# Kernel optimization log

Hardware: AMD Instinct MI355X
Metric: run time of the kernel (lower is better)

The kernel has to match this reference:

```python
import jax, jax.numpy as jnp
import numpy as np

C = 512
B, W, H = 16, 64, 64
K = 128


def setup_inputs() -> dict:
    key = jax.random.key(0)
    ks = jax.random.split(key, 17)
    s = 0.02
    inp = {
        "x1": jax.random.normal(ks[0], (B, C, W, H), jnp.float32),
        "y1": jax.random.normal(ks[1], (B, K, C), jnp.float32),
        "x2": jax.random.normal(ks[2], (B, C, W, H), jnp.float32),
        "y2": jax.random.normal(ks[3], (B, K, C), jnp.float32),
        # 1x1 conv weights stored as [out, in]
        "wq1": jax.random.normal(ks[4], (C // 4, C), jnp.float32) * s,
        "bq1": jnp.zeros((C // 4,), jnp.float32),
        "wq2": jax.random.normal(ks[5], (C // 4, C), jnp.float32) * s,
        "bq2": jnp.zeros((C // 4,), jnp.float32),
        "wk1": jax.random.normal(ks[6], (C // 2, C), jnp.float32) * s,
        "bk1": jnp.zeros((C // 2,), jnp.float32),
        "wk2": jax.random.normal(ks[7], (C // 2, C), jnp.float32) * s,
        "bk2": jnp.zeros((C // 2,), jnp.float32),
        "wv1": jax.random.normal(ks[8], (C, C), jnp.float32) * s,
        "bv1": jnp.zeros((C,), jnp.float32),
        "wv2": jax.random.normal(ks[9], (C, C), jnp.float32) * s,
        "bv2": jnp.zeros((C,), jnp.float32),
        "scale": jnp.ones((1,), jnp.float32) * 0.5,  # nn.Parameter(zeros) would kill grads; nonzero for testing
    }
    return inp


def reference(x1, y1, x2, y2, wq1, bq1, wq2, bq2, wk1, bk1, wk2, bk2,
              wv1, bv1, wv2, bv2, scale):
    b, c, w, h = x1.shape
    n = w * h
    # 1x1 convs == channel-wise linear maps
    q1 = jnp.einsum('bcwh,dc->bdwh', x1, wq1) + bq1[None, :, None, None]
    q2 = jnp.einsum('bcwh,dc->bdwh', x2, wq2) + bq2[None, :, None, None]
    # concat along channels -> [B, C/2, N] -> [B, N, C/2]
    q = jnp.concatenate([q1, q2], axis=1).reshape(b, c // 2, n).transpose(0, 2, 1)
    k1 = y1 @ wk1.T + bk1  # [B, K, C/2]
    k2 = y2 @ wk2.T + bk2
    v1 = y1 @ wv1.T + bv1  # [B, K, C]
    v2 = y2 @ wv2.T + bv2
    e1 = jnp.einsum('bnd,bkd->bnk', q, k1)  # [B, N, K]
    e2 = jnp.einsum('bnd,bkd->bnk', q, k2)
    attn = jax.nn.softmax(jnp.abs(e1 - e2), axis=-1)
    # out = value^T @ attn^T : [B, C, N]
    o1 = jnp.einsum('bkc,bnk->bcn', v1, attn).reshape(b, c, w, h)
    o2 = jnp.einsum('bkc,bnk->bcn', v2, attn).reshape(b, c, w, h)
    out1 = scale[0] * o1 + x1
    out2 = scale[0] * o2 + x2
    return out1, out2
```

## Files before the change

kernel.cpp:

```cpp
#include <hip/hip_runtime.h>

typedef unsigned short u16;
typedef __attribute__((ext_vector_type(8))) short short8v;
typedef __attribute__((ext_vector_type(4))) float floatx4;

#define B_ 16
#define C_ 512
#define N_ 4096
#define K_ 128

__device__ __forceinline__ float bf2f(u16 u) {
    unsigned int x = ((unsigned int)u) << 16;
    return __builtin_bit_cast(float, x);
}
__device__ __forceinline__ u16 f2bf(float f) {
    unsigned int u = __builtin_bit_cast(unsigned int, f);
    u = u + 0x7FFFu + ((u >> 16) & 1u);
    return (u16)(u >> 16);
}

__global__ void conv_all(const float* __restrict__ y1, const float* __restrict__ y2,
                         const float* __restrict__ wk1, const float* __restrict__ wk2,
                         const float* __restrict__ wv1, const float* __restrict__ wv2,
                         const float* __restrict__ wq1, const float* __restrict__ wq2,
                         u16* y1b, u16* y2b, u16* wk1b, u16* wk2b, u16* wv1b, u16* wv2b,
                         u16* wq1t, u16* wq2t) {
    int tid = blockIdx.x * 256 + threadIdx.x;
    const int SY = B_ * K_ * C_;
    const int SWK = 256 * 512;
    const int SWV = 512 * 512;
    const int SQ = 128 * 512;
    int base = 2*SY + 2*SWK + 2*SWV;
    if (tid < base) {
        const float* src; u16* dst; int off;
        if (tid < SY)                 { src = y1;  dst = y1b;  off = tid; }
        else if (tid < 2*SY)          { src = y2;  dst = y2b;  off = tid - SY; }
        else if (tid < 2*SY+SWK)      { src = wk1; dst = wk1b; off = tid - 2*SY; }
        else if (tid < 2*SY+2*SWK)    { src = wk2; dst = wk2b; off = tid - 2*SY - SWK; }
        else if (tid < 2*SY+2*SWK+SWV){ src = wv1; dst = wv1b; off = tid - 2*SY - 2*SWK; }
        else                          { src = wv2; dst = wv2b; off = tid - 2*SY - 2*SWK - SWV; }
        dst[off] = f2bf(src[off]);
    } else {
        int e = tid - base;
        const float* s = (e >= SQ) ? wq2 : wq1;
        u16* d = (e >= SQ) ? wq2t : wq1t;
        e &= (SQ - 1);
        int dd = e >> 9;
        int c = e & 511;
        d[c * 128 + dd] = f2bf(s[dd * 512 + c]);
    }
}

__global__ void gemm_gkgv(const u16* __restrict__ y1b, const u16* __restrict__ y2b,
                          const u16* __restrict__ wk1b, const u16* __restrict__ wk2b,
                          const u16* __restrict__ wv1b, const u16* __restrict__ wv2b,
                          const float* __restrict__ bk1, const float* __restrict__ bk2,
                          const float* __restrict__ bv1, const float* __restrict__ bv2,
                          u16* k1b, u16* k2b, u16* vt1, u16* vt2) {
    int l = threadIdx.x;
    int id = blockIdx.x;
    const u16 *A, *Bt; const float* bias; u16* outp;
    int m0, n0, po; bool bias_m;
    if (id < 256) {
        int bx = id & 1, by = (id >> 1) & 3, z = id >> 3;
        int b = z >> 1, which = z & 1;
        A = (which ? y2b : y1b) + (size_t)b * K_ * C_;
        Bt = which ? wk2b : wk1b;
        bias = which ? bk2 : bk1;
        outp = (which ? k2b : k1b) + (size_t)b * K_ * 256;
        m0 = bx * 64; n0 = by * 64; po = 256; bias_m = false;
    } else {
        int id2 = id - 256;
        int bx = id2 & 7, by = (id2 >> 3) & 1, z = id2 >> 4;
        int b = z >> 1, which = z & 1;
        A = which ? wv2b : wv1b;
        Bt = (which ? y2b : y1b) + (size_t)b * K_ * C_;
        bias = which ? bv2 : bv1;
        outp = (which ? vt2 : vt1) + (size_t)b * C_ * K_;
        m0 = bx * 64; n0 = by * 64; po = 128; bias_m = true;
    }
    floatx4 acc[4][4] = {};
    for (int ch = 0; ch < 16; ++ch) {
        int koff = ch * 32 + (l >> 4) * 8;
        short8v a[4], wv[4];
#pragma unroll
        for (int mf = 0; mf < 4; ++mf) a[mf] = *(const short8v*)(A + (size_t)(m0 + mf*16 + (l & 15)) * 512 + koff);
#pragma unroll
        for (int nf = 0; nf < 4; ++nf) wv[nf] = *(const short8v*)(Bt + (size_t)(n0 + nf*16 + (l & 15)) * 512 + koff);
#pragma unroll
        for (int mf = 0; mf < 4; ++mf)
#pragma unroll
            for (int nf = 0; nf < 4; ++nf)
                acc[mf][nf] = __builtin_amdgcn_mfma_f32_16x16x32_bf16(a[mf], wv[nf], acc[mf][nf], 0, 0, 0);
    }
#pragma unroll
    for (int mf = 0; mf < 4; ++mf)
#pragma unroll
        for (int nf = 0; nf < 4; ++nf)
#pragma unroll
            for (int rg = 0; rg < 4; ++rg) {
                int m = m0 + mf*16 + (l >> 4)*4 + rg;
                int n = n0 + nf*16 + (l & 15);
                outp[(size_t)m * po + n] = f2bf(acc[mf][nf][rg] + (bias_m ? bias[m] : bias[n]));
            }
}

__global__ void kd_sub(const u16* __restrict__ k1b, const u16* __restrict__ k2b,
                       u16* kd) {
    int tid = blockIdx.x * 256 + threadIdx.x;
    kd[tid] = f2bf(bf2f(k1b[tid]) - bf2f(k2b[tid]));
}

__global__ void ebd_k(const u16* __restrict__ kd,
                      const float* __restrict__ bq1, const float* __restrict__ bq2,
                      float* ebd) {
    int tid = blockIdx.x * 256 + threadIdx.x;
    const u16* kb = kd + (size_t)tid * 256;
    float s = 0.f;
    for (int d = 0; d < 128; ++d) s += bq1[d] * bf2f(kb[d]);
    for (int d = 0; d < 128; ++d) s += bq2[d] * bf2f(kb[128 + d]);
    ebd[tid] = s;
}

__global__ void gemm_gkk(const u16* __restrict__ kd,
                         const u16* __restrict__ wq1t, const u16* __restrict__ wq2t,
                         u16* kkd1, u16* kkd2) {
    int l = threadIdx.x;
    int z = blockIdx.z; int b = z >> 1; int which = z & 1;
    const u16* A = kd + (size_t)b * K_ * 256 + which * 128;
    const u16* Wt = which ? wq2t : wq1t;
    u16* outp = (which ? kkd2 : kkd1) + (size_t)b * K_ * C_;
    int m0 = blockIdx.x * 64, n0 = blockIdx.y * 64;
    floatx4 acc[4][4] = {};
    for (int ch = 0; ch < 4; ++ch) {
        int koff = ch * 32 + (l >> 4) * 8;
        short8v a[4], wv[4];
#pragma unroll
        for (int mf = 0; mf < 4; ++mf) a[mf] = *(const short8v*)(A + (size_t)(m0 + mf*16 + (l & 15)) * 256 + koff);
#pragma unroll
        for (int nf = 0; nf < 4; ++nf) wv[nf] = *(const short8v*)(Wt + (size_t)(n0 + nf*16 + (l & 15)) * 128 + koff);
#pragma unroll
        for (int mf = 0; mf < 4; ++mf)
#pragma unroll
            for (int nf = 0; nf < 4; ++nf)
                acc[mf][nf] = __builtin_amdgcn_mfma_f32_16x16x32_bf16(a[mf], wv[nf], acc[mf][nf], 0, 0, 0);
    }
#pragma unroll
    for (int mf = 0; mf < 4; ++mf)
#pragma unroll
        for (int nf = 0; nf < 4; ++nf)
#pragma unroll
            for (int rg = 0; rg < 4; ++rg) {
                int m = m0 + mf*16 + (l >> 4)*4 + rg;
                int n = n0 + nf*16 + (l & 15);
                outp[(size_t)m * C_ + n] = f2bf(acc[mf][nf][rg]);
            }
}

__global__ __launch_bounds__(256, 2)
void e_attn(const float* __restrict__ x1, const float* __restrict__ x2,
            const u16* __restrict__ kkd1, const u16* __restrict__ kkd2,
            const float* __restrict__ ebd, u16* __restrict__ attnb) {
    __shared__ u16 xT[2][128 * 64];
    __shared__ u16 kkS[2][128 * 64];

    int id = blockIdx.x;
    int sw = ((id & 7) << 6) | (id >> 3);
    int b = sw >> 5;
    int n0 = (sw & 31) * 128;
    int t = threadIdx.x, w = t >> 6, l = t & 63;

    const float* xs[2] = { x1 + (size_t)b * C_ * N_, x2 + (size_t)b * C_ * N_ };
    const u16* kkp[2] = { kkd1 + (size_t)b * K_ * C_, kkd2 + (size_t)b * K_ * C_ };

    floatx4 ed[2][8] = {};

    float xA0[16], xA1[16], xB0[16], xB1[16];
    short8v kvA[4], kvB[4];

    auto SLOAD = [&](int s, float (&v0)[16], float (&v1)[16], short8v (&kv)[4]) {
        int h = s >> 3, c0 = (s & 7) * 64;
        const float* xp = xs[h] + (size_t)(c0 + w * 16) * N_ + n0 + 2 * l;
#pragma unroll
        for (int j = 0; j < 16; ++j) {
            float2 f = *(const float2*)(xp + (size_t)j * N_);
            v0[j] = f.x; v1[j] = f.y;
        }
        const u16* kp = kkp[h] + c0;
#pragma unroll
        for (int i = 0; i < 4; ++i) {
            int gi = i * 256 + t;
            kv[i] = *(const short8v*)(kp + (size_t)(gi >> 3) * 512 + (gi & 7) * 8);
        }
    };
    auto SWRITE = [&](int buf, float (&v0)[16], float (&v1)[16], short8v (&kv)[4]) {
        short8v p00, p01, p10, p11;
#pragma unroll
        for (int j = 0; j < 8; ++j) {
            p00[j] = (short)f2bf(v0[j]);  p01[j] = (short)f2bf(v0[j + 8]);
            p10[j] = (short)f2bf(v1[j]);  p11[j] = (short)f2bf(v1[j + 8]);
        }
        u16* xb = xT[buf];
        int row0 = 2 * l, sz = l & 7;
        *(short8v*)&xb[row0 * 64 + 8 * ((w * 2) ^ sz)] = p00;
        *(short8v*)&xb[row0 * 64 + 8 * ((w * 2 + 1) ^ sz)] = p01;
        *(short8v*)&xb[(row0 + 1) * 64 + 8 * ((w * 2) ^ sz)] = p10;
        *(short8v*)&xb[(row0 + 1) * 64 + 8 * ((w * 2 + 1) ^ sz)] = p11;
        u16* kb = kkS[buf];
#pragma unroll
        for (int i = 0; i < 4; ++i) {
            int gi = i * 256 + t;
            int key = gi >> 3, g = gi & 7;
            *(short8v*)&kb[key * 64 + 8 * (g ^ (key & 7))] = kv[i];
        }
    };
    auto COMPUTE = [&](int buf) {
        u16* xb = xT[buf]; u16* kb = kkS[buf];
#pragma unroll
        for (int cc = 0; cc < 2; ++cc) {
            short8v a[2];
#pragma unroll
            for (int mf = 0; mf < 2; ++mf) {
                int row = w * 32 + mf * 16 + (l & 15);
                int g = cc * 4 + (l >> 4);
                a[mf] = *(const short8v*)&xb[row * 64 + 8 * (g ^ ((row >> 1) & 7))];
            }
#pragma unroll
            for (int kf = 0; kf < 8; ++kf) {
                int key = kf * 16 + (l & 15);
                int g = cc * 4 + (l >> 4);
                short8v bb = *(const short8v*)&kb[key * 64 + 8 * (g ^ (key & 7))];
#pragma unroll
                for (int mf = 0; mf < 2; ++mf)
                    ed[mf][kf] = __builtin_amdgcn_mfma_f32_16x16x32_bf16(a[mf], bb, ed[mf][kf], 0, 0, 0);
            }
        }
    };

    SLOAD(0, xA0, xA1, kvA);
    SWRITE(0, xA0, xA1, kvA);
    SLOAD(1, xB0, xB1, kvB);
#pragma unroll
    for (int rr = 0; rr < 8; ++rr) {
        int sA = 2 * rr, sB = 2 * rr + 1;
        __syncthreads();
        COMPUTE(0);
        SWRITE(1, xB0, xB1, kvB);
        if (sA + 2 <= 15) SLOAD(sA + 2, xA0, xA1, kvA);
        __syncthreads();
        COMPUTE(1);
        if (sB + 1 <= 15) SWRITE(0, xA0, xA1, kvA);
        if (sB + 2 <= 15) SLOAD(sB + 2, xB0, xB1, kvB);
    }

    float ebv[8];
#pragma unroll
    for (int kf = 0; kf < 8; ++kf) ebv[kf] = ebd[b * 128 + kf * 16 + (l & 15)];
#pragma unroll
    for (int mf = 0; mf < 2; ++mf)
#pragma unroll
        for (int kf = 0; kf < 8; ++kf)
#pragma unroll
            for (int rg = 0; rg < 4; ++rg)
                ed[mf][kf][rg] = fabsf(ed[mf][kf][rg] + ebv[kf]);

    float mx[2][4], sm[2][4];
#pragma unroll
    for (int mf = 0; mf < 2; ++mf)
#pragma unroll
        for (int rg = 0; rg < 4; ++rg) {
            float m = fmaxf(ed[mf][0][rg], ed[mf][1][rg]);
            m = fmaxf(m, fmaxf(ed[mf][2][rg], ed[mf][3][rg]));
            m = fmaxf(m, fmaxf(ed[mf][4][rg], ed[mf][5][rg]));
            m = fmaxf(m, fmaxf(ed[mf][6][rg], ed[mf][7][rg]));
            mx[mf][rg] = m;
        }
#pragma unroll
    for (int st = 1; st < 16; st <<= 1)
#pragma unroll
        for (int mf = 0; mf < 2; ++mf)
#pragma unroll
            for (int rg = 0; rg < 4; ++rg)
                mx[mf][rg] = fmaxf(mx[mf][rg], __shfl_xor(mx[mf][rg], st));
#pragma unroll
    for (int mf = 0; mf < 2; ++mf)
#pragma unroll
        for (int rg = 0; rg < 4; ++rg) sm[mf][rg] = 0.f;
#pragma unroll
    for (int mf = 0; mf < 2; ++mf)
#pragma unroll
        for (int kf = 0; kf < 8; ++kf)
#pragma unroll
            for (int rg = 0; rg < 4; ++rg) {
                float e = __expf(ed[mf][kf][rg] - mx[mf][rg]);
                ed[mf][kf][rg] = e;
                sm[mf][rg] += e;
            }
#pragma unroll
    for (int st = 1; st < 16; st <<= 1)
#pragma unroll
        for (int mf = 0; mf < 2; ++mf)
#pragma unroll
            for (int rg = 0; rg < 4; ++rg)
                sm[mf][rg] += __shfl_xor(sm[mf][rg], st);
#pragma unroll
    for (int mf = 0; mf < 2; ++mf)
#pragma unroll
        for (int rg = 0; rg < 4; ++rg) sm[mf][rg] = 1.0f / sm[mf][rg];

    u16* ap = attnb + ((size_t)(b * N_ + n0)) * 128;
#pragma unroll
    for (int mf = 0; mf < 2; ++mf)
#pragma unroll
        for (int rg = 0; rg < 4; ++rg) {
            int row = w * 32 + mf * 16 + (l >> 4) * 4 + rg;
#pragma unroll
            for (int kf = 0; kf < 8; ++kf) {
                int col = kf * 16 + (l & 15);
                ap[(size_t)row * 128 + col] = f2bf(ed[mf][kf][rg] * sm[mf][rg]);
            }
        }
}

__global__ __launch_bounds__(256, 2)
void pv_attn(const float* __restrict__ x1, const float* __restrict__ x2,
             const u16* __restrict__ vt1, const u16* __restrict__ vt2,
             const u16* __restrict__ attnb, const float* __restrict__ scale_p,
             float* __restrict__ out1, float* __restrict__ out2) {
    __shared__ u16 As[128 * 128];

    int id = blockIdx.x;
    int sw = ((id & 7) << 9) | (id >> 3);
    int b = sw >> 8;
    int ct = (sw >> 5) & 7;
    int pt = sw & 31;
    int n0 = pt * 128;
    int cb = ct * 128;
    int oi = cb >> 9;
    int cbl = cb & 511;
    int t = threadIdx.x, w = t >> 6, l = t & 63;

    const float sc = scale_p[0];
    const u16* vt = (oi ? vt2 : vt1) + (size_t)b * C_ * K_;
    const float* xr = (oi ? x2 : x1) + (size_t)b * C_ * N_;
    float* op = (oi ? out2 : out1) + (size_t)b * C_ * N_;

    const u16* ap = attnb + ((size_t)(b * N_ + n0)) * 128;
#pragma unroll
    for (int p = 0; p < 8; ++p) {
        int gi = p * 256 + t;
        int px = gi >> 4, g = gi & 15;
        short8v v = *(const short8v*)(ap + (size_t)gi * 8);
        *(short8v*)&As[px * 128 + 8 * (g ^ (px & 15))] = v;
    }

    short8v vf[2][4];
#pragma unroll
    for (int mf = 0; mf < 2; ++mf)
#pragma unroll
        for (int kc = 0; kc < 4; ++kc)
            vf[mf][kc] = *(const short8v*)(vt + (size_t)(cbl + w * 32 + mf * 16 + (l & 15)) * K_ + kc * 32 + (l >> 4) * 8);

    float rs[2][4][8];
#pragma unroll
    for (int mf = 0; mf < 2; ++mf)
#pragma unroll
        for (int rg = 0; rg < 4; ++rg) {
            const float* rp = xr + (size_t)(cbl + w * 32 + mf * 16 + (l >> 4) * 4 + rg) * N_ + n0 + (l & 15);
#pragma unroll
            for (int nf = 0; nf < 8; ++nf)
                rs[mf][rg][nf] = rp[nf * 16];
        }
    __syncthreads();

    floatx4 o[2][8] = {};
#pragma unroll
    for (int kc = 0; kc < 4; ++kc) {
#pragma unroll
        for (int nf = 0; nf < 8; ++nf) {
            int row = nf * 16 + (l & 15);
            int g = kc * 4 + (l >> 4);
            short8v bb = *(const short8v*)&As[row * 128 + 8 * (g ^ (row & 15))];
#pragma unroll
            for (int mf = 0; mf < 2; ++mf)
                o[mf][nf] = __builtin_amdgcn_mfma_f32_16x16x32_bf16(vf[mf][kc], bb, o[mf][nf], 0, 0, 0);
        }
    }

#pragma unroll
    for (int mf = 0; mf < 2; ++mf)
#pragma unroll
        for (int rg = 0; rg < 4; ++rg) {
            float* wp = op + (size_t)(cbl + w * 32 + mf * 16 + (l >> 4) * 4 + rg) * N_ + n0 + (l & 15);
#pragma unroll
            for (int nf = 0; nf < 8; ++nf)
                wp[nf * 16] = sc * o[mf][nf][rg] + rs[mf][rg][nf];
        }
}

extern "C" void kernel_launch(void* const* d_in, const int* in_sizes, int n_in,
                              void* d_out, int out_size, void* d_ws, size_t ws_size,
                              hipStream_t stream) {
    const float* x1 = (const float*)d_in[0];
    const float* y1 = (const float*)d_in[1];
    const float* x2 = (const float*)d_in[2];
    const float* y2 = (const float*)d_in[3];
    const float* wq1 = (const float*)d_in[4];
    const float* bq1 = (const float*)d_in[5];
    const float* wq2 = (const float*)d_in[6];
    const float* bq2 = (const float*)d_in[7];
    const float* wk1 = (const float*)d_in[8];
    const float* bk1 = (const float*)d_in[9];
    const float* wk2 = (const float*)d_in[10];
    const float* bk2 = (const float*)d_in[11];
    const float* wv1 = (const float*)d_in[12];
    const float* bv1 = (const float*)d_in[13];
    const float* wv2 = (const float*)d_in[14];
    const float* bv2 = (const float*)d_in[15];
    const float* scale = (const float*)d_in[16];

    char* ws = (char*)d_ws;
    u16* y1b  = (u16*)(ws + 0);
    u16* y2b  = (u16*)(ws + 2097152);
    u16* wk1b = (u16*)(ws + 4194304);
    u16* wk2b = (u16*)(ws + 4456448);
    u16* wv1b = (u16*)(ws + 4718592);
    u16* wv2b = (u16*)(ws + 5242880);
    u16* wq1t = (u16*)(ws + 5767168);
    u16* wq2t = (u16*)(ws + 5898240);
    u16* k1b  = (u16*)(ws + 6029312);
    u16* k2b  = (u16*)(ws + 7077888);
    u16* kd   = (u16*)(ws + 8126464);
    u16* kkd1 = (u16*)(ws + 9175040);
    u16* kkd2 = (u16*)(ws + 11272192);
    u16* vt1  = (u16*)(ws + 13369344);
    u16* vt2  = (u16*)(ws + 15466496);
    float* ebd = (float*)(ws + 17563648);
    u16* attnb = (u16*)(ws + 17571840);

    float* out1 = (float*)d_out;
    float* out2 = out1 + (size_t)B_ * C_ * N_;

    hipLaunchKernelGGL(conv_all, dim3(11776), dim3(256), 0, stream,
                       y1, y2, wk1, wk2, wv1, wv2, wq1, wq2,
                       y1b, y2b, wk1b, wk2b, wv1b, wv2b, wq1t, wq2t);
    hipLaunchKernelGGL(gemm_gkgv, dim3(768), dim3(64), 0, stream,
                       y1b, y2b, wk1b, wk2b, wv1b, wv2b, bk1, bk2, bv1, bv2,
                       k1b, k2b, vt1, vt2);
    hipLaunchKernelGGL(kd_sub, dim3(2048), dim3(256), 0, stream, k1b, k2b, kd);
    hipLaunchKernelGGL(ebd_k, dim3(8), dim3(256), 0, stream, kd, bq1, bq2, ebd);
    hipLaunchKernelGGL(gemm_gkk, dim3(2, 8, 32), dim3(64), 0, stream,
                       kd, wq1t, wq2t, kkd1, kkd2);
    hipLaunchKernelGGL(e_attn, dim3(512), dim3(256), 0, stream,
                       x1, x2, kkd1, kkd2, ebd, attnb);
    hipLaunchKernelGGL(pv_attn, dim3(4096), dim3(256), 0, stream,
                       x1, x2, vt1, vt2, attnb, scale, out1, out2);
}
```

Measured before the change: 236.4 us.

## Fuse key difference into K GEMM and restructure pv_attn for higher occupancy

The K projection GEMM now computes both k1 and k2 accumulators in one block and writes their difference directly, removing the separate kd_sub kernel and the k1b/k2b intermediates. pv_attn processes its two M-fragments sequentially, loading residual x values at store time instead of prefetching them into registers, and raises launch bounds to 4 blocks per SM. The aim is to cut one launch plus intermediate traffic and to raise occupancy in the dominant output kernel. The cost is doubled accumulator registers in the fused GEMM and the loss of the early residual prefetch, which exposes the x load latency.

```diff
diff --git a/kernel.cpp b/kernel.cpp
--- a/kernel.cpp
+++ b/kernel.cpp
@@ -51,64 +51,89 @@
     }
 }
 
-__global__ void gemm_gkgv(const u16* __restrict__ y1b, const u16* __restrict__ y2b,
-                          const u16* __restrict__ wk1b, const u16* __restrict__ wk2b,
-                          const u16* __restrict__ wv1b, const u16* __restrict__ wv2b,
-                          const float* __restrict__ bk1, const float* __restrict__ bk2,
-                          const float* __restrict__ bv1, const float* __restrict__ bv2,
-                          u16* k1b, u16* k2b, u16* vt1, u16* vt2) {
+__global__ void gemm_gkdgv(const u16* __restrict__ y1b, const u16* __restrict__ y2b,
+                           const u16* __restrict__ wk1b, const u16* __restrict__ wk2b,
+                           const u16* __restrict__ wv1b, const u16* __restrict__ wv2b,
+                           const float* __restrict__ bk1, const float* __restrict__ bk2,
+                           const float* __restrict__ bv1, const float* __restrict__ bv2,
+                           u16* kd, u16* vt1, u16* vt2) {
     int l = threadIdx.x;
     int id = blockIdx.x;
-    const u16 *A, *Bt; const float* bias; u16* outp;
-    int m0, n0, po; bool bias_m;
-    if (id < 256) {
-        int bx = id & 1, by = (id >> 1) & 3, z = id >> 3;
-        int b = z >> 1, which = z & 1;
-        A = (which ? y2b : y1b) + (size_t)b * K_ * C_;
-        Bt = which ? wk2b : wk1b;
-        bias = which ? bk2 : bk1;
-        outp = (which ? k2b : k1b) + (size_t)b * K_ * 256;
-        m0 = bx * 64; n0 = by * 64; po = 256; bias_m = false;
+    if (id < 128) {
+        int b = id >> 3, r = id & 7;
+        int m0 = (r & 1) * 64;
+        int n0 = (r >> 1) * 64;
+        const u16* A1 = y1b + (size_t)b * K_ * C_;
+        const u16* A2 = y2b + (size_t)b * K_ * C_;
+        u16* outp = kd + (size_t)b * K_ * 256;
+        floatx4 acc1[4][4] = {}, acc2[4][4] = {};
+        for (int ch = 0; ch < 16; ++ch) {
+            int koff = ch * 32 + (l >> 4) * 8;
+            short8v a1[4], a2[4], w1[4], w2[4];
+#pragma unroll
+            for (int mf = 0; mf < 4; ++mf) {
+                size_t ro = (size_t)(m0 + mf*16 + (l & 15)) * 512 + koff;
+                a1[mf] = *(const short8v*)(A1 + ro);
+                a2[mf] = *(const short8v*)(A2 + ro);
+            }
+#pragma unroll
+            for (int nf = 0; nf < 4; ++nf) {
+                size_t ro = (size_t)(n0 + nf*16 + (l & 15)) * 512 + koff;
+                w1[nf] = *(const short8v*)(wk1b + ro);
+                w2[nf] = *(const short8v*)(wk2b + ro);
+            }
+#pragma unroll
+            for (int mf = 0; mf < 4; ++mf)
+#pragma unroll
+                for (int nf = 0; nf < 4; ++nf) {
+                    acc1[mf][nf] = __builtin_amdgcn_mfma_f32_16x16x32_bf16(a1[mf], w1[nf], acc1[mf][nf], 0, 0, 0);
+                    acc2[mf][nf] = __builtin_amdgcn_mfma_f32_16x16x32_bf16(a2[mf], w2[nf], acc2[mf][nf], 0, 0, 0);
+                }
+        }
+#pragma unroll
+        for (int mf = 0; mf < 4; ++mf)
+#pragma unroll
+            for (int nf = 0; nf < 4; ++nf)
+#pragma unroll
+                for (int rg = 0; rg < 4; ++rg) {
+                    int m = m0 + mf*16 + (l >> 4)*4 + rg;
+                    int n = n0 + nf*16 + (l & 15);
+                    outp[(size_t)m * 256 + n] = f2bf(acc1[mf][nf][rg] - acc2[mf][nf][rg] + bk1[n] - bk2[n]);
+                }
     } else {
-        int id2 = id - 256;
+        int id2 = id - 128;
         int bx = id2 & 7, by = (id2 >> 3) & 1, z = id2 >> 4;
         int b = z >> 1, which = z & 1;
-        A = which ? wv2b : wv1b;
-        Bt = (which ? y2b : y1b) + (size_t)b * K_ * C_;
-        bias = which ? bv2 : bv1;
-        outp = (which ? vt2 : vt1) + (size_t)b * C_ * K_;
-        m0 = bx * 64; n0 = by * 64; po = 128; bias_m = true;
-    }
-    floatx4 acc[4][4] = {};
-    for (int ch = 0; ch < 16; ++ch) {
-        int koff = ch * 32 + (l >> 4) * 8;
-        short8v a[4], wv[4];
-#pragma unroll
-        for (int mf = 0; mf < 4; ++mf) a[mf] = *(const short8v*)(A + (size_t)(m0 + mf*16 + (l & 15)) * 512 + koff);
-#pragma unroll
-        for (int nf = 0; nf < 4; ++nf) wv[nf] = *(const short8v*)(Bt + (size_t)(n0 + nf*16 + (l & 15)) * 512 + koff);
+        const u16* A = which ? wv2b : wv1b;
+        const u16* Bt = (which ? y2b : y1b) + (size_t)b * K_ * C_;
+        const float* bias = which ? bv2 : bv1;
+        u16* outp = (which ? vt2 : vt1) + (size_t)b * C_ * K_;
+        int m0 = bx * 64, n0 = by * 64;
+        floatx4 acc[4][4] = {};
+        for (int ch = 0; ch < 16; ++ch) {
+            int koff = ch * 32 + (l >> 4) * 8;
+            short8v a[4], wv[4];
+#pragma unroll
+            for (int mf = 0; mf < 4; ++mf) a[mf] = *(const short8v*)(A + (size_t)(m0 + mf*16 + (l & 15)) * 512 + koff);
+#pragma unroll
+            for (int nf = 0; nf < 4; ++nf) wv[nf] = *(const short8v*)(Bt + (size_t)(n0 + nf*16 + (l & 15)) * 512 + koff);
+#pragma unroll
+            for (int mf = 0; mf < 4; ++mf)
+#pragma unroll
+                for (int nf = 0; nf < 4; ++nf)
+                    acc[mf][nf] = __builtin_amdgcn_mfma_f32_16x16x32_bf16(a[mf], wv[nf], acc[mf][nf], 0, 0, 0);
+        }
 #pragma unroll
         for (int mf = 0; mf < 4; ++mf)
 #pragma unroll
             for (int nf = 0; nf < 4; ++nf)
-                acc[mf][nf] = __builtin_amdgcn_mfma_f32_16x16x32_bf16(a[mf], wv[nf], acc[mf][nf], 0, 0, 0);
-    }
-#pragma unroll
-    for (int mf = 0; mf < 4; ++mf)
-#pragma unroll
-        for (int nf = 0; nf < 4; ++nf)
-#pragma unroll
-            for (int rg = 0; rg < 4; ++rg) {
-                int m = m0 + mf*16 + (l >> 4)*4 + rg;
-                int n = n0 + nf*16 + (l & 15);
-                outp[(size_t)m * po + n] = f2bf(acc[mf][nf][rg] + (bias_m ? bias[m] : bias[n]));
-            }
-}
-
-__global__ void kd_sub(const u16* __restrict__ k1b, const u16* __restrict__ k2b,
-                       u16* kd) {
-    int tid = blockIdx.x * 256 + threadIdx.x;
-    kd[tid] = f2bf(bf2f(k1b[tid]) - bf2f(k2b[tid]));
+#pragma unroll
+                for (int rg = 0; rg < 4; ++rg) {
+                    int m = m0 + mf*16 + (l >> 4)*4 + rg;
+                    int n = n0 + nf*16 + (l & 15);
+                    outp[(size_t)m * 128 + n] = f2bf(acc[mf][nf][rg] + bias[m]);
+                }
+    }
 }
 
 __global__ void ebd_k(const u16* __restrict__ kd,
@@ -322,7 +347,7 @@
         }
 }
 
-__global__ __launch_bounds__(256, 2)
+__global__ __launch_bounds__(256, 4)
 void pv_attn(const float* __restrict__ x1, const float* __restrict__ x2,
              const u16* __restrict__ vt1, const u16* __restrict__ vt2,
              const u16* __restrict__ attnb, const float* __restrict__ scale_p,
@@ -353,49 +378,33 @@
         short8v v = *(const short8v*)(ap + (size_t)gi * 8);
         *(short8v*)&As[px * 128 + 8 * (g ^ (px & 15))] = v;
     }
-
-    short8v vf[2][4];
-#pragma unroll
-    for (int mf = 0; mf < 2; ++mf)
+    __syncthreads();
+
+#pragma unroll
+    for (int mf = 0; mf < 2; ++mf) {
+        short8v vf[4];
 #pragma unroll
         for (int kc = 0; kc < 4; ++kc)
-            vf[mf][kc] = *(const short8v*)(vt + (size_t)(cbl + w * 32 + mf * 16 + (l & 15)) * K_ + kc * 32 + (l >> 4) * 8);
-
-    float rs[2][4][8];
-#pragma unroll
-    for (int mf = 0; mf < 2; ++mf)
+            vf[kc] = *(const short8v*)(vt + (size_t)(cbl + w * 32 + mf * 16 + (l & 15)) * K_ + kc * 32 + (l >> 4) * 8);
+        floatx4 o[8] = {};
+#pragma unroll
+        for (int kc = 0; kc < 4; ++kc) {
+#pragma unroll
+            for (int nf = 0; nf < 8; ++nf) {
+                int row = nf * 16 + (l & 15);
+                int g = kc * 4 + (l >> 4);
+                short8v bb = *(const short8v*)&As[row * 128 + 8 * (g ^ (row & 15))];
+                o[nf] = __builtin_amdgcn_mfma_f32_16x16x32_bf16(vf[kc], bb, o[nf], 0, 0, 0);
+            }
+        }
 #pragma unroll
         for (int rg = 0; rg < 4; ++rg) {
-            const float* rp = xr + (size_t)(cbl + w * 32 + mf * 16 + (l >> 4) * 4 + rg) * N_ + n0 + (l & 15);
+            size_t rowoff = (size_t)(cbl + w * 32 + mf * 16 + (l >> 4) * 4 + rg) * N_ + n0 + (l & 15);
 #pragma unroll
             for (int nf = 0; nf < 8; ++nf)
-                rs[mf][rg][nf] = rp[nf * 16];
-        }
-    __syncthreads();
-
-    floatx4 o[2][8] = {};
-#pragma unroll
-    for (int kc = 0; kc < 4; ++kc) {
-#pragma unroll
-        for (int nf = 0; nf < 8; ++nf) {
-            int row = nf * 16 + (l & 15);
-            int g = kc * 4 + (l >> 4);
-            short8v bb = *(const short8v*)&As[row * 128 + 8 * (g ^ (row & 15))];
-#pragma unroll
-            for (int mf = 0; mf < 2; ++mf)
-                o[mf][nf] = __builtin_amdgcn_mfma_f32_16x16x32_bf16(vf[mf][kc], bb, o[mf][nf], 0, 0, 0);
-        }
-    }
-
-#pragma unroll
-    for (int mf = 0; mf < 2; ++mf)
-#pragma unroll
-        for (int rg = 0; rg < 4; ++rg) {
-            float* wp = op + (size_t)(cbl + w * 32 + mf * 16 + (l >> 4) * 4 + rg) * N_ + n0 + (l & 15);
-#pragma unroll
-            for (int nf = 0; nf < 8; ++nf)
-                wp[nf * 16] = sc * o[mf][nf][rg] + rs[mf][rg][nf];
-        }
+                op[rowoff + nf * 16] = sc * o[nf][rg] + xr[rowoff + nf * 16];
+        }
+    }
 }
 
 extern "C" void kernel_launch(void* const* d_in, const int* in_sizes, int n_in,
@@ -428,8 +437,6 @@
     u16* wv2b = (u16*)(ws + 5242880);
     u16* wq1t = (u16*)(ws + 5767168);
     u16* wq2t = (u16*)(ws + 5898240);
-    u16* k1b  = (u16*)(ws + 6029312);
-    u16* k2b  = (u16*)(ws + 7077888);
     u16* kd   = (u16*)(ws + 8126464);
     u16* kkd1 = (u16*)(ws + 9175040);
     u16* kkd2 = (u16*)(ws + 11272192);
@@ -444,10 +451,9 @@
     hipLaunchKernelGGL(conv_all, dim3(11776), dim3(256), 0, stream,
                        y1, y2, wk1, wk2, wv1, wv2, wq1, wq2,
                        y1b, y2b, wk1b, wk2b, wv1b, wv2b, wq1t, wq2t);
-    hipLaunchKernelGGL(gemm_gkgv, dim3(768), dim3(64), 0, stream,
+    hipLaunchKernelGGL(gemm_gkdgv, dim3(640), dim3(64), 0, stream,
                        y1b, y2b, wk1b, wk2b, wv1b, wv2b, bk1, bk2, bv1, bv2,
-                       k1b, k2b, vt1, vt2);
-    hipLaunchKernelGGL(kd_sub, dim3(2048), dim3(256), 0, stream, k1b, k2b, kd);
+                       kd, vt1, vt2);
     hipLaunchKernelGGL(ebd_k, dim3(8), dim3(256), 0, stream, kd, bq1, bq2, ebd);
     hipLaunchKernelGGL(gemm_gkk, dim3(2, 8, 32), dim3(64), 0, stream,
                        kd, wq1t, wq2t, kkd1, kkd2);
```

Result: slower. 305.6 us (+29.3%).
